# Kernel tuning notes

Measured on AMD Instinct MI355X. Metric: run time of the kernel, lower is better.

Reference implementation:

```python
import jax, jax.numpy as jnp
import numpy as np

N = 10000      # num_nodes
E = 320000     # num_edges
B = 8          # batch
S = 12         # seq_length
H = 64         # hidden_channels
HEADS = 4
C = H // HEADS # per-head dim = 16
L = 3          # num_layers
P = 3          # pred_length
EPS = 1e-5


def setup_inputs():
    key = jax.random.key(0)
    ks = jax.random.split(key, 20)
    g = lambda k, sh, s=0.05: jax.random.normal(k, sh, dtype=jnp.float32) * s
    return {
        "x": jax.random.normal(ks[0], (B, S, N), dtype=jnp.float32),
        "edge_index": jax.random.randint(ks[1], (2, E), 0, N, dtype=jnp.int64),
        "in_W": g(ks[2], (S, H), 0.2), "in_b": g(ks[3], (H,)),
        "Wq": g(ks[4], (L, H, H), 0.1), "bq": g(ks[5], (L, H)),
        "Wk": g(ks[6], (L, H, H), 0.1), "bk": g(ks[7], (L, H)),
        "Wv": g(ks[8], (L, H, H), 0.1), "bv": g(ks[9], (L, H)),
        "Wsk": g(ks[10], (L, H, H), 0.1), "bsk": g(ks[11], (L, H)),
        "ln_g": jnp.ones((H,), jnp.float32), "ln_b": jnp.zeros((H,), jnp.float32),
        "out_W": g(ks[12], (H, P), 0.1), "out_b": g(ks[13], (P,)),
    }


def _layer_norm(x, g, b):
    mu = x.mean(-1, keepdims=True)
    var = ((x - mu) ** 2).mean(-1, keepdims=True)
    return (x - mu) * jax.lax.rsqrt(var + EPS) * g + b


def _transformer_conv(x, src, dst, Wq, bq, Wk, bk, Wv, bv, Wsk, bsk):
    # x: [N, H]; PyG TransformerConv, concat=True, root_weight=True, beta=False
    n = x.shape[0]
    q = (x @ Wq + bq).reshape(n, HEADS, C)
    k = (x @ Wk + bk).reshape(n, HEADS, C)
    v = (x @ Wv + bv).reshape(n, HEADS, C)
    # messages flow src -> dst; attention logits per edge per head
    logits = (q[dst] * k[src]).sum(-1) / np.sqrt(C)           # [E, HEADS]
    m = jax.ops.segment_max(logits, dst, num_segments=n)       # [N, HEADS]
    e = jnp.exp(logits - m[dst])
    den = jax.ops.segment_sum(e, dst, num_segments=n)          # [N, HEADS]
    a = e / den[dst]                                           # [E, HEADS]
    agg = jax.ops.segment_sum(a[..., None] * v[src], dst, num_segments=n)
    return agg.reshape(n, H) + x @ Wsk + bsk


def reference(x, edge_index, in_W, in_b, Wq, bq, Wk, bk, Wv, bv, Wsk, bsk,
              ln_g, ln_b, out_W, out_b):
    src, dst = edge_index[0], edge_index[1]
    h = jnp.einsum('bsn,sh->bnh', x, in_W) + in_b              # [B, N, H]
    for l in range(L):
        conv = jax.vmap(lambda xb: _transformer_conv(
            xb, src, dst, Wq[l], bq[l], Wk[l], bk[l],
            Wv[l], bv[l], Wsk[l], bsk[l]))(h)
        h = _layer_norm(h + conv, ln_g, ln_b)                  # dropout: eval mode
    out = h @ out_W + out_b                                    # [B, N, P]
    return out.transpose(0, 2, 1)                              # [B, P, N]
```

## Files before the change

kernel.cpp:

```cpp
#include <hip/hip_runtime.h>
#include <hip/hip_bf16.h>
#include <math.h>

#define NN 10000
#define EE 320000
#define BB 8
#define SS 12
#define PP 3
#define LL 3
#define BN (BB*NN)
#define CSR_CAP (EE + 16*NN + 64)
#define QSCL (0.25f * 1.44269504f)

typedef __attribute__((ext_vector_type(8))) short bf8_t;
typedef __attribute__((ext_vector_type(4))) float f4_t;

__device__ __forceinline__ float bf2f(unsigned short u) {
    unsigned int x = ((unsigned int)u) << 16;
    return __builtin_bit_cast(float, x);
}
__device__ __forceinline__ unsigned short f2bf(float f) {
    unsigned int u = __builtin_bit_cast(unsigned int, f);
    u += 0x7FFF + ((u >> 16) & 1);
    return (unsigned short)(u >> 16);
}
__device__ __forceinline__ unsigned short f2h(float f) {
    _Float16 h = (_Float16)f;
    return __builtin_bit_cast(unsigned short, h);
}
__device__ __forceinline__ float dot2(unsigned a, unsigned b, float c) {
    float d;
    asm("v_dot2_f32_f16 %0, %1, %2, %3" : "=v"(d) : "v"(a), "v"(b), "v"(c));
    return d;
}
template<int CTRL>
__device__ __forceinline__ float dppadd(float x) {
    int t = __builtin_amdgcn_update_dpp(0, __builtin_bit_cast(int, x), CTRL, 0xF, 0xF, true);
    return x + __builtin_bit_cast(float, t);
}
#define QX1 0xB1
#define QX2 0x4E
#define RR4 0x124
#define RR8 0x128
__device__ __forceinline__ float quad_sum(float x) {
    x = dppadd<QX1>(x); x = dppadd<QX2>(x); return x;
}
__device__ __forceinline__ float row_sum(float x) {
    x = dppadd<QX1>(x); x = dppadd<QX2>(x);
    x = dppadd<RR4>(x); x = dppadd<RR8>(x); return x;
}

__global__ __launch_bounds__(256) void k_count(const int* __restrict__ ei, int* __restrict__ cnt,
                                               const float* __restrict__ Wq, const float* __restrict__ Wk,
                                               const float* __restrict__ Wv, const float* __restrict__ Ws,
                                               const float* __restrict__ bq, const float* __restrict__ bk,
                                               const float* __restrict__ bv, const float* __restrict__ bs,
                                               unsigned short* __restrict__ wtb, float* __restrict__ bprep) {
    int e = blockIdx.x * 256 + threadIdx.x;
    if (e < EE) atomicAdd(&cnt[ei[EE + e]], 1);
    if (e < LL * 4 * 64 * 64) {
        int l = e >> 14; int j = (e >> 12) & 3; int col = (e >> 6) & 63; int k = e & 63;
        const float* W = (j == 0 ? Wq : j == 1 ? Wk : j == 2 ? Wv : Ws) + l * 4096;
        float v = W[k * 64 + col];
        if (j == 0) v *= QSCL;
        wtb[e] = f2bf(v);
    }
    if (e < LL * 4 * 64) {
        int l = e >> 8; int j = (e >> 6) & 3; int c = e & 63;
        const float* bsrc = (j == 0 ? bq : j == 1 ? bk : j == 2 ? bv : bs) + l * 64;
        bprep[e] = bsrc[c] * (j == 0 ? QSCL : 1.0f);
    }
}

__global__ __launch_bounds__(1024) void k_scan(int* __restrict__ cnt,
                                               int* __restrict__ rp,
                                               int* __restrict__ degv) {
    __shared__ int ssum[1024];
    int t = threadIdx.x;
    int base = t * 10;
    int loc[10];
    int s = 0;
#pragma unroll
    for (int j = 0; j < 10; ++j) {
        int i = base + j;
        int d = (i < NN) ? cnt[i] : 0;
        loc[j] = d;
        s += (d + 15) & ~15;
    }
    ssum[t] = s;
    __syncthreads();
    for (int off = 1; off < 1024; off <<= 1) {
        int v = (t >= off) ? ssum[t - off] : 0;
        __syncthreads();
        ssum[t] += v;
        __syncthreads();
    }
    int run = ssum[t] - s;
#pragma unroll
    for (int j = 0; j < 10; ++j) {
        int i = base + j;
        if (i < NN) {
            rp[i]   = run;
            degv[i] = loc[j];
            cnt[i]  = run;
            run += (loc[j] + 15) & ~15;
        }
    }
}

__global__ __launch_bounds__(256) void k_fill(const int* __restrict__ ei, int* __restrict__ cursor,
                                              int* __restrict__ csr) {
    int e = blockIdx.x * 256 + threadIdx.x;
    if (e >= EE) return;
    int dst = ei[EE + e];
    int pos = atomicAdd(&cursor[dst], 1);
    csr[pos] = ei[e] << 7;
}

__global__ __launch_bounds__(256, 4) void k_gemm(const float* __restrict__ x,
                                                 const float* __restrict__ inW,
                                                 const float* __restrict__ inb,
                                                 int first,
                                                 unsigned short* hb,
                                                 float* h,
                                                 const unsigned short* __restrict__ wtb,
                                                 const float* __restrict__ bprep,
                                                 unsigned short* __restrict__ qh,
                                                 unsigned short* __restrict__ kh,
                                                 unsigned short* __restrict__ vb) {
    int tid = threadIdx.x;
    int l = tid & 63, w = tid >> 6;
    int row0 = blockIdx.x * 64;
    int colb = l & 15, kg = l >> 4, rquad = kg;

    if (first) {
        int c = tid & 63;
        int rb = tid >> 6;
        for (int j = 0; j < 16; ++j) {
            int row = row0 + rb + j * 4;
            int b = row / NN;
            int n = row - b * NN;
            float s = inb[c];
#pragma unroll
            for (int t = 0; t < SS; ++t)
                s += x[((size_t)b * SS + t) * NN + n] * inW[t * 64 + c];
            h[(size_t)row * 64 + c]  = s;
            hb[(size_t)row * 64 + c] = f2bf(s);
        }
        __syncthreads();
    }

    const unsigned short* wb = wtb + (size_t)w * 4096;
    bf8_t wfr[2][4];
#pragma unroll
    for (int ks = 0; ks < 2; ++ks)
#pragma unroll
        for (int ct = 0; ct < 4; ++ct)
            wfr[ks][ct] = *(const bf8_t*)(wb + (ct * 16 + colb) * 64 + ks * 32 + kg * 8);
    float4 biasv[4];
#pragma unroll
    for (int ct = 0; ct < 4; ++ct)
        biasv[ct] = *(const float4*)(bprep + w * 64 + ct * 16 + rquad * 4);

#pragma unroll
    for (int rt = 0; rt < 4; ++rt) {
        bf8_t hfr[2];
#pragma unroll
        for (int ks = 0; ks < 2; ++ks)
            hfr[ks] = *(const bf8_t*)(hb + (size_t)(row0 + rt * 16 + colb) * 64 + ks * 32 + kg * 8);
        f4_t acc[4];
#pragma unroll
        for (int ct = 0; ct < 4; ++ct) acc[ct] = (f4_t){0.f, 0.f, 0.f, 0.f};
#pragma unroll
        for (int ks = 0; ks < 2; ++ks)
#pragma unroll
            for (int ct = 0; ct < 4; ++ct)
                acc[ct] = __builtin_amdgcn_mfma_f32_16x16x32_bf16(wfr[ks][ct], hfr[ks], acc[ct], 0, 0, 0);

        size_t rowoff = (size_t)(row0 + rt * 16 + colb) * 64;
#pragma unroll
        for (int ct = 0; ct < 4; ++ct) {
            int c0 = ct * 16 + rquad * 4;
            float v0 = acc[ct][0] + biasv[ct].x;
            float v1 = acc[ct][1] + biasv[ct].y;
            float v2 = acc[ct][2] + biasv[ct].z;
            float v3 = acc[ct][3] + biasv[ct].w;
            if (w == 0) {
                ushort4 st = {f2h(v0), f2h(v1), f2h(v2), f2h(v3)};
                *(ushort4*)(qh + rowoff + c0) = st;
            } else if (w == 1) {
                ushort4 st = {f2h(v0), f2h(v1), f2h(v2), f2h(v3)};
                *(ushort4*)(kh + rowoff + c0) = st;
            } else if (w == 2) {
                ushort4 st = {f2bf(v0), f2bf(v1), f2bf(v2), f2bf(v3)};
                *(ushort4*)(vb + rowoff + c0) = st;
            } else {
                float4 hv = *(float4*)(h + rowoff + c0);
                hv.x += v0; hv.y += v1; hv.z += v2; hv.w += v3;
                *(float4*)(h + rowoff + c0) = hv;
            }
        }
    }
}

__global__ __launch_bounds__(256, 8) void k_attn_ln(const unsigned short* __restrict__ qh,
                                                    const unsigned short* __restrict__ kh,
                                                    const unsigned short* __restrict__ vb,
                                                    const int* __restrict__ rp,
                                                    const int* __restrict__ degv,
                                                    const int* __restrict__ csr,
                                                    const float* __restrict__ lng,
                                                    const float* __restrict__ lnb,
                                                    float* __restrict__ h,
                                                    unsigned short* __restrict__ hb,
                                                    const float* __restrict__ oW,
                                                    const float* __restrict__ ob,
                                                    float* __restrict__ out) {
    int b    = blockIdx.x & 7;
    int n    = ((blockIdx.x >> 3) << 2) | __builtin_amdgcn_readfirstlane(threadIdx.x >> 6);
    int lane = threadIdx.x & 63;
    int lg   = lane & 15;
    int grp  = lane >> 4;
    size_t wid = (size_t)b * NN + n;

    const char* kbase = (const char*)kh + (size_t)b * NN * 128;
    const char* vbase = (const char*)vb + (size_t)b * NN * 128;
    int lgoff = lg * 8;

    uint2 qp = ((const uint2*)qh)[wid * 16 + lg];

    int e0 = rp[n], deg = degv[n];
    int nf  = deg >> 4;
    int rem = deg & 15;
    float den0 = 0.f, den1 = 0.f;
    float4 av0 = {0.f, 0.f, 0.f, 0.f}, av1 = {0.f, 0.f, 0.f, 0.f};

    int e = e0;
    for (int f = 0; f < nf; ++f, e += 16) {
        int c0 = csr[e + grp];
        int c1 = csr[e + 4 + grp];
        int c2 = csr[e + 8 + grp];
        int c3 = csr[e + 12 + grp];
        unsigned o0 = (unsigned)(c0 + lgoff), o1 = (unsigned)(c1 + lgoff);
        unsigned o2 = (unsigned)(c2 + lgoff), o3 = (unsigned)(c3 + lgoff);
        uint2 k0 = *(const uint2*)(kbase + o0);
        uint2 k1 = *(const uint2*)(kbase + o1);
        uint2 k2 = *(const uint2*)(kbase + o2);
        uint2 k3 = *(const uint2*)(kbase + o3);
        ushort4 v0 = *(const ushort4*)(vbase + o0);
        ushort4 v1 = *(const ushort4*)(vbase + o1);
        ushort4 v2 = *(const ushort4*)(vbase + o2);
        ushort4 v3 = *(const ushort4*)(vbase + o3);

        float d0 = dot2(k0.y, qp.y, dot2(k0.x, qp.x, 0.f));
        float d1 = dot2(k1.y, qp.y, dot2(k1.x, qp.x, 0.f));
        float d2 = dot2(k2.y, qp.y, dot2(k2.x, qp.x, 0.f));
        float d3 = dot2(k3.y, qp.y, dot2(k3.x, qp.x, 0.f));
        d0 = quad_sum(d0); d1 = quad_sum(d1);
        d2 = quad_sum(d2); d3 = quad_sum(d3);

        float w0 = __builtin_amdgcn_exp2f(d0);
        float w1 = __builtin_amdgcn_exp2f(d1);
        float w2 = __builtin_amdgcn_exp2f(d2);
        float w3 = __builtin_amdgcn_exp2f(d3);

        den0 += w0 + w1;
        den1 += w2 + w3;
        av0.x += w0 * bf2f(v0.x) + w1 * bf2f(v1.x);
        av0.y += w0 * bf2f(v0.y) + w1 * bf2f(v1.y);
        av0.z += w0 * bf2f(v0.z) + w1 * bf2f(v1.z);
        av0.w += w0 * bf2f(v0.w) + w1 * bf2f(v1.w);
        av1.x += w2 * bf2f(v2.x) + w3 * bf2f(v3.x);
        av1.y += w2 * bf2f(v2.y) + w3 * bf2f(v3.y);
        av1.z += w2 * bf2f(v2.z) + w3 * bf2f(v3.z);
        av1.w += w2 * bf2f(v2.w) + w3 * bf2f(v3.w);
    }
    if (rem) {
        int c0 = csr[e + grp];
        int c1 = csr[e + 4 + grp];
        int c2 = csr[e + 8 + grp];
        int c3 = csr[e + 12 + grp];
        unsigned o0 = (unsigned)(c0 + lgoff), o1 = (unsigned)(c1 + lgoff);
        unsigned o2 = (unsigned)(c2 + lgoff), o3 = (unsigned)(c3 + lgoff);
        uint2 k0 = *(const uint2*)(kbase + o0);
        uint2 k1 = *(const uint2*)(kbase + o1);
        uint2 k2 = *(const uint2*)(kbase + o2);
        uint2 k3 = *(const uint2*)(kbase + o3);
        ushort4 v0 = *(const ushort4*)(vbase + o0);
        ushort4 v1 = *(const ushort4*)(vbase + o1);
        ushort4 v2 = *(const ushort4*)(vbase + o2);
        ushort4 v3 = *(const ushort4*)(vbase + o3);

        float m0 = (grp      < rem) ? 1.f : 0.f;
        float m1 = (grp + 4  < rem) ? 1.f : 0.f;
        float m2 = (grp + 8  < rem) ? 1.f : 0.f;
        float m3 = (grp + 12 < rem) ? 1.f : 0.f;

        float d0 = dot2(k0.y, qp.y, dot2(k0.x, qp.x, 0.f));
        float d1 = dot2(k1.y, qp.y, dot2(k1.x, qp.x, 0.f));
        float d2 = dot2(k2.y, qp.y, dot2(k2.x, qp.x, 0.f));
        float d3 = dot2(k3.y, qp.y, dot2(k3.x, qp.x, 0.f));
        d0 = quad_sum(d0); d1 = quad_sum(d1);
        d2 = quad_sum(d2); d3 = quad_sum(d3);

        float w0 = m0 * __builtin_amdgcn_exp2f(d0);
        float w1 = m1 * __builtin_amdgcn_exp2f(d1);
        float w2 = m2 * __builtin_amdgcn_exp2f(d2);
        float w3 = m3 * __builtin_amdgcn_exp2f(d3);

        den0 += w0 + w1;
        den1 += w2 + w3;
        av0.x += w0 * bf2f(v0.x) + w1 * bf2f(v1.x);
        av0.y += w0 * bf2f(v0.y) + w1 * bf2f(v1.y);
        av0.z += w0 * bf2f(v0.z) + w1 * bf2f(v1.z);
        av0.w += w0 * bf2f(v0.w) + w1 * bf2f(v1.w);
        av1.x += w2 * bf2f(v2.x) + w3 * bf2f(v3.x);
        av1.y += w2 * bf2f(v2.y) + w3 * bf2f(v3.y);
        av1.z += w2 * bf2f(v2.z) + w3 * bf2f(v3.z);
        av1.w += w2 * bf2f(v2.w) + w3 * bf2f(v3.w);
    }

    float den = den0 + den1;
    float4 av = {av0.x + av1.x, av0.y + av1.y, av0.z + av1.z, av0.w + av1.w};

#pragma unroll
    for (int off = 16; off <= 32; off <<= 1) {
        den  += __shfl_xor(den, off);
        av.x += __shfl_xor(av.x, off); av.y += __shfl_xor(av.y, off);
        av.z += __shfl_xor(av.z, off); av.w += __shfl_xor(av.w, off);
    }
    float inv = (den > 0.f) ? __builtin_amdgcn_rcpf(den) : 0.f;

    float4 h4 = ((const float4*)h)[wid * 16 + lg];
    float4 x4;
    x4.x = h4.x + av.x * inv; x4.y = h4.y + av.y * inv;
    x4.z = h4.z + av.z * inv; x4.w = h4.w + av.w * inv;

    float s = row_sum(x4.x + x4.y + x4.z + x4.w);
    float mu = s * (1.f / 64.f);
    float4 dx;
    dx.x = x4.x - mu; dx.y = x4.y - mu; dx.z = x4.z - mu; dx.w = x4.w - mu;
    float vs = row_sum(dx.x * dx.x + dx.y * dx.y + dx.z * dx.z + dx.w * dx.w);
    float r = __builtin_amdgcn_rsqf(vs * (1.f / 64.f) + 1e-5f);

    float4 g4 = ((const float4*)lng)[lg];
    float4 b4 = ((const float4*)lnb)[lg];
    float4 o4;
    o4.x = dx.x * r * g4.x + b4.x; o4.y = dx.y * r * g4.y + b4.y;
    o4.z = dx.z * r * g4.z + b4.z; o4.w = dx.w * r * g4.w + b4.w;

    if (oW) {
        int c0 = lg * 4;
        float t0 = o4.x * oW[(c0+0)*3+0] + o4.y * oW[(c0+1)*3+0] + o4.z * oW[(c0+2)*3+0] + o4.w * oW[(c0+3)*3+0];
        float t1 = o4.x * oW[(c0+0)*3+1] + o4.y * oW[(c0+1)*3+1] + o4.z * oW[(c0+2)*3+1] + o4.w * oW[(c0+3)*3+1];
        float t2 = o4.x * oW[(c0+0)*3+2] + o4.y * oW[(c0+1)*3+2] + o4.z * oW[(c0+2)*3+2] + o4.w * oW[(c0+3)*3+2];
        t0 = row_sum(t0); t1 = row_sum(t1); t2 = row_sum(t2);
        if (lane == 0) {
            out[((size_t)b * PP + 0) * NN + n] = t0 + ob[0];
            out[((size_t)b * PP + 1) * NN + n] = t1 + ob[1];
            out[((size_t)b * PP + 2) * NN + n] = t2 + ob[2];
        }
    } else if (lane < 16) {
        ((float4*)h)[wid * 16 + lg] = o4;
        ushort4 hu = {f2bf(o4.x), f2bf(o4.y), f2bf(o4.z), f2bf(o4.w)};
        ((ushort4*)hb)[wid * 16 + lg] = hu;
    }
}

extern "C" void kernel_launch(void* const* d_in, const int* in_sizes, int n_in,
                              void* d_out, int out_size, void* d_ws, size_t ws_size,
                              hipStream_t stream) {
    const float* x    = (const float*)d_in[0];
    const int*   ei   = (const int*)  d_in[1];
    const float* inW  = (const float*)d_in[2];
    const float* inb  = (const float*)d_in[3];
    const float* Wq   = (const float*)d_in[4];
    const float* bq   = (const float*)d_in[5];
    const float* Wk   = (const float*)d_in[6];
    const float* bk   = (const float*)d_in[7];
    const float* Wv   = (const float*)d_in[8];
    const float* bv   = (const float*)d_in[9];
    const float* Wsk  = (const float*)d_in[10];
    const float* bsk  = (const float*)d_in[11];
    const float* lng  = (const float*)d_in[12];
    const float* lnb  = (const float*)d_in[13];
    const float* outW = (const float*)d_in[14];
    const float* outb = (const float*)d_in[15];
    float* out = (float*)d_out;

    float* h    = (float*)d_ws;
    unsigned short* hb = (unsigned short*)(h + (size_t)BN * 64);
    unsigned short* qh = hb + (size_t)BN * 64;
    unsigned short* kh = qh + (size_t)BN * 64;
    unsigned short* vb = kh + (size_t)BN * 64;
    int* rp      = (int*)(vb + (size_t)BN * 64);
    int* degv    = rp + NN;
    int* cursor  = degv + NN;
    int* csr     = cursor + NN;
    unsigned short* wtb = (unsigned short*)(csr + CSR_CAP);
    float* bprep = (float*)(wtb + LL * 4 * 64 * 64);

    hipMemsetAsync(cursor, 0, (NN + CSR_CAP) * sizeof(int), stream);
    k_count<<<(EE + 255) / 256, 256, 0, stream>>>(ei, cursor, Wq, Wk, Wv, Wsk,
                                                  bq, bk, bv, bsk, wtb, bprep);
    k_scan <<<1, 1024, 0, stream>>>(cursor, rp, degv);
    k_fill <<<(EE + 255) / 256, 256, 0, stream>>>(ei, cursor, csr);

    for (int l = 0; l < LL; ++l) {
        k_gemm<<<BN / 64, 256, 0, stream>>>(x, inW, inb, (l == 0) ? 1 : 0, hb, h,
                                            wtb + (size_t)l * 4 * 4096,
                                            bprep + (size_t)l * 4 * 64, qh, kh, vb);
        k_attn_ln<<<BN / 4, 256, 0, stream>>>(qh, kh, vb, rp, degv, csr,
                                              lng, lnb, h, hb,
                                              (l == LL - 1) ? outW : nullptr, outb, out);
    }
}
```

Before: 347.0 us.

## Interleave K and V into one fp16 buffer and use mixed-precision FMA

K and V are written into a single interleaved fp16 array, 4 K values then 4 V values per 16-byte chunk. Each gathered neighbour now needs one 16-byte load instead of two 8-byte loads from separate arrays, and the CSR indices are read as one int4 per lane group. V switches from bf16 to fp16, so v_fma_mix can fold the conversion into the accumulate. Edge assignment within each 16-edge group changes from strided to contiguous, and fp16 V gives a different value range and precision than bf16.

```diff
diff --git a/kernel.cpp b/kernel.cpp
--- a/kernel.cpp
+++ b/kernel.cpp
@@ -31,6 +31,18 @@
 __device__ __forceinline__ float dot2(unsigned a, unsigned b, float c) {
     float d;
     asm("v_dot2_f32_f16 %0, %1, %2, %3" : "=v"(d) : "v"(a), "v"(b), "v"(c));
+    return d;
+}
+__device__ __forceinline__ float fma_mixlo(unsigned v, float w, float acc) {
+    float d;
+    asm("v_fma_mix_f32 %0, %1, %2, %3 op_sel_hi:[1,0,0]"
+        : "=v"(d) : "v"(v), "v"(w), "v"(acc));
+    return d;
+}
+__device__ __forceinline__ float fma_mixhi(unsigned v, float w, float acc) {
+    float d;
+    asm("v_fma_mix_f32 %0, %1, %2, %3 op_sel:[1,0,0] op_sel_hi:[1,0,0]"
+        : "=v"(d) : "v"(v), "v"(w), "v"(acc));
     return d;
 }
 template<int CTRL>
@@ -114,7 +126,7 @@
     if (e >= EE) return;
     int dst = ei[EE + e];
     int pos = atomicAdd(&cursor[dst], 1);
-    csr[pos] = ei[e] << 7;
+    csr[pos] = ei[e] << 8;
 }
 
 __global__ __launch_bounds__(256, 4) void k_gemm(const float* __restrict__ x,
@@ -126,8 +138,7 @@
                                                  const unsigned short* __restrict__ wtb,
                                                  const float* __restrict__ bprep,
                                                  unsigned short* __restrict__ qh,
-                                                 unsigned short* __restrict__ kh,
-                                                 unsigned short* __restrict__ vb) {
+                                                 unsigned short* __restrict__ kv) {
     int tid = threadIdx.x;
     int l = tid & 63, w = tid >> 6;
     int row0 = blockIdx.x * 64;
@@ -177,7 +188,8 @@
             for (int ct = 0; ct < 4; ++ct)
                 acc[ct] = __builtin_amdgcn_mfma_f32_16x16x32_bf16(wfr[ks][ct], hfr[ks], acc[ct], 0, 0, 0);
 
-        size_t rowoff = (size_t)(row0 + rt * 16 + colb) * 64;
+        int rowid = row0 + rt * 16 + colb;
+        size_t rowoff = (size_t)rowid * 64;
 #pragma unroll
         for (int ct = 0; ct < 4; ++ct) {
             int c0 = ct * 16 + rquad * 4;
@@ -190,10 +202,10 @@
                 *(ushort4*)(qh + rowoff + c0) = st;
             } else if (w == 1) {
                 ushort4 st = {f2h(v0), f2h(v1), f2h(v2), f2h(v3)};
-                *(ushort4*)(kh + rowoff + c0) = st;
+                *(ushort4*)(kv + (size_t)rowid * 128 + ((c0 >> 2) << 3)) = st;
             } else if (w == 2) {
-                ushort4 st = {f2bf(v0), f2bf(v1), f2bf(v2), f2bf(v3)};
-                *(ushort4*)(vb + rowoff + c0) = st;
+                ushort4 st = {f2h(v0), f2h(v1), f2h(v2), f2h(v3)};
+                *(ushort4*)(kv + (size_t)rowid * 128 + ((c0 >> 2) << 3) + 4) = st;
             } else {
                 float4 hv = *(float4*)(h + rowoff + c0);
                 hv.x += v0; hv.y += v1; hv.z += v2; hv.w += v3;
@@ -204,8 +216,7 @@
 }
 
 __global__ __launch_bounds__(256, 8) void k_attn_ln(const unsigned short* __restrict__ qh,
-                                                    const unsigned short* __restrict__ kh,
-                                                    const unsigned short* __restrict__ vb,
+                                                    const unsigned short* __restrict__ kv,
                                                     const int* __restrict__ rp,
                                                     const int* __restrict__ degv,
                                                     const int* __restrict__ csr,
@@ -223,9 +234,8 @@
     int grp  = lane >> 4;
     size_t wid = (size_t)b * NN + n;
 
-    const char* kbase = (const char*)kh + (size_t)b * NN * 128;
-    const char* vbase = (const char*)vb + (size_t)b * NN * 128;
-    int lgoff = lg * 8;
+    const char* kvbase = (const char*)kv + (size_t)b * NN * 256;
+    int lgoff = lg * 16;
 
     uint2 qp = ((const uint2*)qh)[wid * 16 + lg];
 
@@ -237,25 +247,20 @@
 
     int e = e0;
     for (int f = 0; f < nf; ++f, e += 16) {
-        int c0 = csr[e + grp];
-        int c1 = csr[e + 4 + grp];
-        int c2 = csr[e + 8 + grp];
-        int c3 = csr[e + 12 + grp];
-        unsigned o0 = (unsigned)(c0 + lgoff), o1 = (unsigned)(c1 + lgoff);
-        unsigned o2 = (unsigned)(c2 + lgoff), o3 = (unsigned)(c3 + lgoff);
-        uint2 k0 = *(const uint2*)(kbase + o0);
-        uint2 k1 = *(const uint2*)(kbase + o1);
-        uint2 k2 = *(const uint2*)(kbase + o2);
-        uint2 k3 = *(const uint2*)(kbase + o3);
-        ushort4 v0 = *(const ushort4*)(vbase + o0);
-        ushort4 v1 = *(const ushort4*)(vbase + o1);
-        ushort4 v2 = *(const ushort4*)(vbase + o2);
-        ushort4 v3 = *(const ushort4*)(vbase + o3);
-
-        float d0 = dot2(k0.y, qp.y, dot2(k0.x, qp.x, 0.f));
-        float d1 = dot2(k1.y, qp.y, dot2(k1.x, qp.x, 0.f));
-        float d2 = dot2(k2.y, qp.y, dot2(k2.x, qp.x, 0.f));
-        float d3 = dot2(k3.y, qp.y, dot2(k3.x, qp.x, 0.f));
+        int4 cc = *(const int4*)(csr + e + grp * 4);
+        unsigned o0 = (unsigned)(cc.x + lgoff);
+        unsigned o1 = (unsigned)(cc.y + lgoff);
+        unsigned o2 = (unsigned)(cc.z + lgoff);
+        unsigned o3 = (unsigned)(cc.w + lgoff);
+        uint4 a0 = *(const uint4*)(kvbase + o0);
+        uint4 a1 = *(const uint4*)(kvbase + o1);
+        uint4 a2 = *(const uint4*)(kvbase + o2);
+        uint4 a3 = *(const uint4*)(kvbase + o3);
+
+        float d0 = dot2(a0.y, qp.y, dot2(a0.x, qp.x, 0.f));
+        float d1 = dot2(a1.y, qp.y, dot2(a1.x, qp.x, 0.f));
+        float d2 = dot2(a2.y, qp.y, dot2(a2.x, qp.x, 0.f));
+        float d3 = dot2(a3.y, qp.y, dot2(a3.x, qp.x, 0.f));
         d0 = quad_sum(d0); d1 = quad_sum(d1);
         d2 = quad_sum(d2); d3 = quad_sum(d3);
 
@@ -266,40 +271,36 @@
 
         den0 += w0 + w1;
         den1 += w2 + w3;
-        av0.x += w0 * bf2f(v0.x) + w1 * bf2f(v1.x);
-        av0.y += w0 * bf2f(v0.y) + w1 * bf2f(v1.y);
-        av0.z += w0 * bf2f(v0.z) + w1 * bf2f(v1.z);
-        av0.w += w0 * bf2f(v0.w) + w1 * bf2f(v1.w);
-        av1.x += w2 * bf2f(v2.x) + w3 * bf2f(v3.x);
-        av1.y += w2 * bf2f(v2.y) + w3 * bf2f(v3.y);
-        av1.z += w2 * bf2f(v2.z) + w3 * bf2f(v3.z);
-        av1.w += w2 * bf2f(v2.w) + w3 * bf2f(v3.w);
+        av0.x = fma_mixlo(a0.z, w0, av0.x); av0.x = fma_mixlo(a1.z, w1, av0.x);
+        av0.y = fma_mixhi(a0.z, w0, av0.y); av0.y = fma_mixhi(a1.z, w1, av0.y);
+        av0.z = fma_mixlo(a0.w, w0, av0.z); av0.z = fma_mixlo(a1.w, w1, av0.z);
+        av0.w = fma_mixhi(a0.w, w0, av0.w); av0.w = fma_mixhi(a1.w, w1, av0.w);
+        av1.x = fma_mixlo(a2.z, w2, av1.x); av1.x = fma_mixlo(a3.z, w3, av1.x);
+        av1.y = fma_mixhi(a2.z, w2, av1.y); av1.y = fma_mixhi(a3.z, w3, av1.y);
+        av1.z = fma_mixlo(a2.w, w2, av1.z); av1.z = fma_mixlo(a3.w, w3, av1.z);
+        av1.w = fma_mixhi(a2.w, w2, av1.w); av1.w = fma_mixhi(a3.w, w3, av1.w);
     }
     if (rem) {
-        int c0 = csr[e + grp];
-        int c1 = csr[e + 4 + grp];
-        int c2 = csr[e + 8 + grp];
-        int c3 = csr[e + 12 + grp];
-        unsigned o0 = (unsigned)(c0 + lgoff), o1 = (unsigned)(c1 + lgoff);
-        unsigned o2 = (unsigned)(c2 + lgoff), o3 = (unsigned)(c3 + lgoff);
-        uint2 k0 = *(const uint2*)(kbase + o0);
-        uint2 k1 = *(const uint2*)(kbase + o1);
-        uint2 k2 = *(const uint2*)(kbase + o2);
-        uint2 k3 = *(const uint2*)(kbase + o3);
-        ushort4 v0 = *(const ushort4*)(vbase + o0);
-        ushort4 v1 = *(const ushort4*)(vbase + o1);
-        ushort4 v2 = *(const ushort4*)(vbase + o2);
-        ushort4 v3 = *(const ushort4*)(vbase + o3);
-
-        float m0 = (grp      < rem) ? 1.f : 0.f;
-        float m1 = (grp + 4  < rem) ? 1.f : 0.f;
-        float m2 = (grp + 8  < rem) ? 1.f : 0.f;
-        float m3 = (grp + 12 < rem) ? 1.f : 0.f;
-
-        float d0 = dot2(k0.y, qp.y, dot2(k0.x, qp.x, 0.f));
-        float d1 = dot2(k1.y, qp.y, dot2(k1.x, qp.x, 0.f));
-        float d2 = dot2(k2.y, qp.y, dot2(k2.x, qp.x, 0.f));
-        float d3 = dot2(k3.y, qp.y, dot2(k3.x, qp.x, 0.f));
+        int4 cc = *(const int4*)(csr + e + grp * 4);
+        unsigned o0 = (unsigned)(cc.x + lgoff);
+        unsigned o1 = (unsigned)(cc.y + lgoff);
+        unsigned o2 = (unsigned)(cc.z + lgoff);
+        unsigned o3 = (unsigned)(cc.w + lgoff);
+        uint4 a0 = *(const uint4*)(kvbase + o0);
+        uint4 a1 = *(const uint4*)(kvbase + o1);
+        uint4 a2 = *(const uint4*)(kvbase + o2);
+        uint4 a3 = *(const uint4*)(kvbase + o3);
+
+        int eb = grp * 4;
+        float m0 = (eb + 0 < rem) ? 1.f : 0.f;
+        float m1 = (eb + 1 < rem) ? 1.f : 0.f;
+        float m2 = (eb + 2 < rem) ? 1.f : 0.f;
+        float m3 = (eb + 3 < rem) ? 1.f : 0.f;
+
+        float d0 = dot2(a0.y, qp.y, dot2(a0.x, qp.x, 0.f));
+        float d1 = dot2(a1.y, qp.y, dot2(a1.x, qp.x, 0.f));
+        float d2 = dot2(a2.y, qp.y, dot2(a2.x, qp.x, 0.f));
+        float d3 = dot2(a3.y, qp.y, dot2(a3.x, qp.x, 0.f));
         d0 = quad_sum(d0); d1 = quad_sum(d1);
         d2 = quad_sum(d2); d3 = quad_sum(d3);
 
@@ -310,14 +311,14 @@
 
         den0 += w0 + w1;
         den1 += w2 + w3;
-        av0.x += w0 * bf2f(v0.x) + w1 * bf2f(v1.x);
-        av0.y += w0 * bf2f(v0.y) + w1 * bf2f(v1.y);
-        av0.z += w0 * bf2f(v0.z) + w1 * bf2f(v1.z);
-        av0.w += w0 * bf2f(v0.w) + w1 * bf2f(v1.w);
-        av1.x += w2 * bf2f(v2.x) + w3 * bf2f(v3.x);
-        av1.y += w2 * bf2f(v2.y) + w3 * bf2f(v3.y);
-        av1.z += w2 * bf2f(v2.z) + w3 * bf2f(v3.z);
-        av1.w += w2 * bf2f(v2.w) + w3 * bf2f(v3.w);
+        av0.x = fma_mixlo(a0.z, w0, av0.x); av0.x = fma_mixlo(a1.z, w1, av0.x);
+        av0.y = fma_mixhi(a0.z, w0, av0.y); av0.y = fma_mixhi(a1.z, w1, av0.y);
+        av0.z = fma_mixlo(a0.w, w0, av0.z); av0.z = fma_mixlo(a1.w, w1, av0.z);
+        av0.w = fma_mixhi(a0.w, w0, av0.w); av0.w = fma_mixhi(a1.w, w1, av0.w);
+        av1.x = fma_mixlo(a2.z, w2, av1.x); av1.x = fma_mixlo(a3.z, w3, av1.x);
+        av1.y = fma_mixhi(a2.z, w2, av1.y); av1.y = fma_mixhi(a3.z, w3, av1.y);
+        av1.z = fma_mixlo(a2.w, w2, av1.z); av1.z = fma_mixlo(a3.w, w3, av1.z);
+        av1.w = fma_mixhi(a2.w, w2, av1.w); av1.w = fma_mixhi(a3.w, w3, av1.w);
     }
 
     float den = den0 + den1;
@@ -391,9 +392,8 @@
     float* h    = (float*)d_ws;
     unsigned short* hb = (unsigned short*)(h + (size_t)BN * 64);
     unsigned short* qh = hb + (size_t)BN * 64;
-    unsigned short* kh = qh + (size_t)BN * 64;
-    unsigned short* vb = kh + (size_t)BN * 64;
-    int* rp      = (int*)(vb + (size_t)BN * 64);
+    unsigned short* kv = qh + (size_t)BN * 64;
+    int* rp      = (int*)(kv + (size_t)BN * 128);
     int* degv    = rp + NN;
     int* cursor  = degv + NN;
     int* csr     = cursor + NN;
@@ -409,8 +409,8 @@
     for (int l = 0; l < LL; ++l) {
         k_gemm<<<BN / 64, 256, 0, stream>>>(x, inW, inb, (l == 0) ? 1 : 0, hb, h,
                                             wtb + (size_t)l * 4 * 4096,
-                                            bprep + (size_t)l * 4 * 64, qh, kh, vb);
-        k_attn_ln<<<BN / 4, 256, 0, stream>>>(qh, kh, vb, rp, degv, csr,
+                                            bprep + (size_t)l * 4 * 64, qh, kv);
+        k_attn_ln<<<BN / 4, 256, 0, stream>>>(qh, kv, rp, degv, csr,
                                               lng, lnb, h, hb,
                                               (l == LL - 1) ? outW : nullptr, outb, out);
     }
```

New measurement: 286.5 us. 17.4% less time.
